# Optimization experiments

Hardware: AMD Instinct MI355X
Metric: run time of the kernel (lower is better)

The kernel has to match this reference:

```python
import jax, jax.numpy as jnp
import numpy as np

BATCH, C_IN, H = 16, 32, 224
N_FILT, K = 64, 5


def setup_inputs() -> dict:
    key = jax.random.key(0)
    k1, k2 = jax.random.split(key)
    x = jax.random.normal(k1, (BATCH, C_IN, H, H), dtype=jnp.float32)
    weight = jax.random.normal(k2, (N_FILT, C_IN, K, K), dtype=jnp.float32)
    bias = jnp.zeros((N_FILT,), dtype=jnp.float32)  # torch init: zeros(1) per filter
    return {"x": x, "weight": weight, "bias": bias}


def reference(x, weight, bias):
    # Fully-connected conv layer: stride 1, VALID padding.
    # Equivalent to stacking per-filter sum(x_patch * w) + scalar bias.
    out = jax.lax.conv_general_dilated(
        x, weight,
        window_strides=(1, 1),
        padding='VALID',
        dimension_numbers=('NCHW', 'OIHW', 'NCHW'),
    )
    # per-filter scalar bias broadcast over spatial dims
    return out + bias[None, :, None, None]
```

## Files before the change

### kernel.cpp

```cpp
#include <hip/hip_runtime.h>

#define CI    32
#define IH    224
#define IW    224
#define OHS   220
#define OWS   220
#define NF    64
#define KS    5

#define XCOLS 228
#define CP    36
#define WPD   40
#define XROWS 8
#define NBUFW (KS * NF * WPD)

#define PXW   116
#define RCHK  (PXW * 4)
#define NROWS 8
#define TCHK  (RCHK * NROWS)
#define ROWB  (RCHK * 16)

typedef __attribute__((ext_vector_type(4))) float   f32x4;
typedef __attribute__((ext_vector_type(4))) __bf16  bf16x4;
typedef __attribute__((ext_vector_type(8))) __bf16  bf16x8;

__global__ void repack_w_kernel(const float* __restrict__ w, __bf16* __restrict__ wp) {
  int i = blockIdx.x * 256 + threadIdx.x;
  if (i >= KS * KS * NF * CI) return;
  int c   = i & (CI - 1);
  int f   = (i >> 5) & (NF - 1);
  int tap = i >> 11;
  int kh = tap / KS, kw = tap % KS;
  wp[i] = (__bf16)w[((f * CI + c) * KS + kh) * KS + kw];
}

__global__ __launch_bounds__(256)
void x_transform(const float* __restrict__ x, __bf16* __restrict__ xh) {
  int chunk = blockIdx.x * 256 + threadIdx.x;
  int c8  = (chunk & 3) * 8;
  int pos = chunk >> 2;
  int w   = pos % IW;
  int nh  = pos / IW;
  int n   = nh / IH;
  int h   = nh - n * IH;
  const float* xp = x + ((size_t)n * CI + c8) * (IH * IW) + h * IW + w;
  bf16x8 v;
#pragma unroll
  for (int j = 0; j < 8; ++j) v[j] = (__bf16)xp[(size_t)j * (IH * IW)];
  *(bf16x8*)(xh + (size_t)pos * CI + c8) = v;
}

__global__ __launch_bounds__(256, 2)
void conv_lds(const __bf16* __restrict__ xh, const __bf16* __restrict__ wp,
              const float* __restrict__ bias, float* __restrict__ out) {
  __shared__ __bf16 xs[TCHK * 8];

  const int tid  = threadIdx.x;
  const int lane = tid & 63;
  const int wv   = tid >> 6;
  const int m    = lane & 15;
  const int q    = lane >> 4;

  const int bid = blockIdx.x;
  const int lid = (bid & 7) * 220 + (bid >> 3);
  const int n   = lid / 110;
  const int rem = lid - n * 110;
  const int oh0 = (rem >> 1) * 4;
  const int ow0 = (rem & 1) * 112;

  {
    const __bf16* xb = xh + (((size_t)n * IH + oh0) * IW + ow0) * CI;
    for (int i = wv; i < TCHK / 64; i += 4) {
      int L  = i * 64 + lane;
      int r  = L / RCHK;
      int cr = L - r * RCHK;
      int cs = cr ^ ((cr >> 3) & 3);
      const __bf16* src = xb + (size_t)r * (IW * CI) + cs * 8;
      __builtin_amdgcn_global_load_lds(
          (const __attribute__((address_space(1))) void*)src,
          (__attribute__((address_space(3))) void*)&xs[i * 512], 16, 0, 0);
    }
  }

  int cj[7], rjv[7];
  int boff[7][5];
#pragma unroll
  for (int j = 0; j < 7; ++j) {
    int t  = wv + j * 4;
    int rj = t / 7;
    rjv[j] = rj;
    cj[j]  = (t - rj * 7) * 16;
#pragma unroll
    for (int kw = 0; kw < KS; ++kw) {
      int g = (cj[j] + kw + m) * 4 + q;
      int s = g ^ ((g >> 3) & 3);
      boff[j][kw] = rj * ROWB + s * 16;
    }
  }

  f32x4 acc[28];
#pragma unroll
  for (int i = 0; i < 28; ++i) { f32x4 z = {0.f, 0.f, 0.f, 0.f}; acc[i] = z; }

  const __bf16* wpl = wp + m * CI + q * 8;

  __syncthreads();

  for (int kh = 0; kh < KS; ++kh) {
    const int khb = kh * ROWB;
#pragma unroll
    for (int kw = 0; kw < KS; ++kw) {
      const int tap = kh * KS + kw;
      bf16x8 af[4];
#pragma unroll
      for (int ft = 0; ft < 4; ++ft)
        af[ft] = *(const bf16x8*)(wpl + (size_t)tap * (NF * CI) + ft * 16 * CI);
#pragma unroll
      for (int j = 0; j < 7; ++j) {
        bf16x8 bv = *(const bf16x8*)((const char*)xs + khb + boff[j][kw]);
#pragma unroll
        for (int ft = 0; ft < 4; ++ft)
          acc[j * 4 + ft] =
              __builtin_amdgcn_mfma_f32_16x16x32_bf16(af[ft], bv, acc[j * 4 + ft], 0, 0, 0);
      }
    }
  }

  float bvv[16];
#pragma unroll
  for (int ft = 0; ft < 4; ++ft)
#pragma unroll
    for (int rg = 0; rg < 4; ++rg)
      bvv[ft * 4 + rg] = bias[ft * 16 + q * 4 + rg];

#pragma unroll
  for (int j = 0; j < 7; ++j) {
    int ow = ow0 + cj[j] + m;
    if (ow < OWS) {
      int oh = oh0 + rjv[j];
#pragma unroll
      for (int ft = 0; ft < 4; ++ft)
#pragma unroll
        for (int rg = 0; rg < 4; ++rg) {
          int f = ft * 16 + q * 4 + rg;
          out[(((size_t)n * NF + f) * OHS + oh) * OWS + ow] = acc[j * 4 + ft][rg] + bvv[ft * 4 + rg];
        }
    }
  }
}

template <bool USE_WS>
__global__ __launch_bounds__(512, 1)
void conv_main(const float* __restrict__ x, const float* __restrict__ w,
               const __bf16* __restrict__ wp, const float* __restrict__ bias,
               float* __restrict__ out) {
  __shared__ __bf16 xs[XROWS * XCOLS * CP];
  __shared__ __bf16 wsm[NBUFW];

  const int tid  = threadIdx.x;
  const int lane = tid & 63;
  const int wv   = tid >> 6;
  const int m    = lane & 15;
  const int q    = lane >> 4;

  int bid = blockIdx.x;
  int lid = (bid >> 3) + (bid & 7) * 110;
  const int n   = lid / 55;
  const int oh0 = (lid % 55) * 4;

  {
    const float* xn = x + (size_t)n * CI * IH * IW;
    for (int p = tid; p < XROWS * 56 * 8; p += 512) {
      int pc   = p & 7;
      int pg   = p >> 3;
      int pcol = pg % 56;
      int prow = pg / 56;
      int row  = oh0 + prow;
      f32x4 v0 = *(const f32x4*)(xn + ((size_t)(pc * 4 + 0) * IH + row) * IW + pcol * 4);
      f32x4 v1 = *(const f32x4*)(xn + ((size_t)(pc * 4 + 1) * IH + row) * IW + pcol * 4);
      f32x4 v2 = *(const f32x4*)(xn + ((size_t)(pc * 4 + 2) * IH + row) * IW + pcol * 4);
      f32x4 v3 = *(const f32x4*)(xn + ((size_t)(pc * 4 + 3) * IH + row) * IW + pcol * 4);
#pragma unroll
      for (int dcol = 0; dcol < 4; ++dcol) {
        bf16x4 t;
        t[0] = (__bf16)v0[dcol]; t[1] = (__bf16)v1[dcol];
        t[2] = (__bf16)v2[dcol]; t[3] = (__bf16)v3[dcol];
        *(bf16x4*)&xs[(prow * XCOLS + pcol * 4 + dcol) * CP + pc * 4] = t;
      }
    }
    for (int z = tid; z < XROWS * 4 * CP; z += 512) {
      int rr  = z / (4 * CP);
      int rem = z - rr * (4 * CP);
      xs[(rr * XCOLS + 224) * CP + rem] = (__bf16)0.0f;
    }
  }

  if (USE_WS) {
    for (int i = tid; i < NF * CI * KS / 8; i += 512) {
      int c0 = (i & 3) * 8;
      int f  = (i >> 2) & 63;
      int kw = i >> 8;
      bf16x8 v = *(const bf16x8*)(wp + ((size_t)(0 * KS + kw) * NF + f) * CI + c0);
      *(bf16x8*)&wsm[(kw * NF + f) * WPD + c0] = v;
    }
  } else {
    for (int i = tid; i < KS * NF * CI; i += 512) {
      int c  = i & 31;
      int f  = (i >> 5) & 63;
      int kw = i >> 11;
      wsm[(kw * NF + f) * WPD + c] = (__bf16)w[((f * CI + c) * KS + 0) * KS + kw];
    }
  }
  __syncthreads();

  int rj[7], cbj[7], xoff[7];
#pragma unroll
  for (int j = 0; j < 7; ++j) {
    int t   = wv + j * 8;
    rj[j]   = t / 14;
    cbj[j]  = (t % 14) * 16;
    xoff[j] = (rj[j] * XCOLS + cbj[j] + m) * CP + q * 8;
  }

  f32x4 acc[28];
#pragma unroll
  for (int i = 0; i < 28; ++i) { f32x4 z = {0.f, 0.f, 0.f, 0.f}; acc[i] = z; }

  for (int kh = 0; kh < KS; ++kh) {
    bf16x8 pw[3];
    if (USE_WS && kh < KS - 1) {
#pragma unroll
      for (int it = 0; it < 3; ++it) {
        int e = it * 512 + tid;
        if (e < 1280) {
          int c0 = (e & 3) * 8;
          int f  = (e >> 2) & 63;
          int kw = e >> 8;
          pw[it] = *(const bf16x8*)(wp + ((size_t)((kh + 1) * KS + kw) * NF + f) * CI + c0);
        }
      }
    }

#pragma unroll
    for (int kw = 0; kw < KS; ++kw) {
      bf16x8 af[4];
#pragma unroll
      for (int ft = 0; ft < 4; ++ft)
        af[ft] = *(const bf16x8*)&wsm[(kw * NF + ft * 16 + m) * WPD + q * 8];
#pragma unroll
      for (int j = 0; j < 7; ++j) {
        const __bf16* bp = &xs[xoff[j] + (kh * XCOLS + kw) * CP];
        bf16x4 lo = *(const bf16x4*)bp;
        bf16x4 hi = *(const bf16x4*)(bp + 4);
        bf16x8 bv8 = __builtin_shufflevector(lo, hi, 0, 1, 2, 3, 4, 5, 6, 7);
#pragma unroll
        for (int ft = 0; ft < 4; ++ft)
          acc[j * 4 + ft] =
              __builtin_amdgcn_mfma_f32_16x16x32_bf16(af[ft], bv8, acc[j * 4 + ft], 0, 0, 0);
      }
    }

    if (kh < KS - 1) {
      __syncthreads();
      if (USE_WS) {
#pragma unroll
        for (int it = 0; it < 3; ++it) {
          int e = it * 512 + tid;
          if (e < 1280) {
            int c0 = (e & 3) * 8;
            int f  = (e >> 2) & 63;
            int kw = e >> 8;
            *(bf16x8*)&wsm[(kw * NF + f) * WPD + c0] = pw[it];
          }
        }
      } else {
        for (int i = tid; i < KS * NF * CI; i += 512) {
          int c  = i & 31;
          int f  = (i >> 5) & 63;
          int kw = i >> 11;
          wsm[(kw * NF + f) * WPD + c] =
              (__bf16)w[((f * CI + c) * KS + (kh + 1)) * KS + kw];
        }
      }
      __syncthreads();
    }
  }

  float bvv[16];
#pragma unroll
  for (int ft = 0; ft < 4; ++ft)
#pragma unroll
    for (int rg = 0; rg < 4; ++rg)
      bvv[ft * 4 + rg] = bias[ft * 16 + q * 4 + rg];

#pragma unroll
  for (int j = 0; j < 7; ++j) {
    int ow = cbj[j] + m;
    if (ow < OWS) {
      int oh = oh0 + rj[j];
#pragma unroll
      for (int ft = 0; ft < 4; ++ft) {
#pragma unroll
        for (int rg = 0; rg < 4; ++rg) {
          int f = ft * 16 + q * 4 + rg;
          out[(((size_t)n * NF + f) * OHS + oh) * OWS + ow] = acc[j * 4 + ft][rg] + bvv[ft * 4 + rg];
        }
      }
    }
  }
}

extern "C" void kernel_launch(void* const* d_in, const int* in_sizes, int n_in,
                              void* d_out, int out_size, void* d_ws, size_t ws_size,
                              hipStream_t stream) {
  const float* x    = (const float*)d_in[0];
  const float* w    = (const float*)d_in[1];
  const float* bias = (const float*)d_in[2];
  float* out = (float*)d_out;

  const int    NW = KS * KS * NF * CI;
  const size_t WB = (size_t)NW * sizeof(__bf16);
  const size_t XB = (size_t)16 * IH * IW * CI * sizeof(__bf16);

  if (ws_size >= XB + WB) {
    __bf16* xhp = (__bf16*)d_ws;
    __bf16* wp  = (__bf16*)((char*)d_ws + XB);
    repack_w_kernel<<<(NW + 255) / 256, 256, 0, stream>>>(w, wp);
    x_transform<<<(16 * IH * IW * 4) / 256, 256, 0, stream>>>(x, xhp);
    conv_lds<<<1760, 256, 0, stream>>>(xhp, wp, bias, out);
  } else if (ws_size >= WB) {
    __bf16* wp = (__bf16*)d_ws;
    repack_w_kernel<<<(NW + 255) / 256, 256, 0, stream>>>(w, wp);
    conv_main<true><<<880, 512, 0, stream>>>(x, w, wp, bias, out);
  } else {
    conv_main<false><<<880, 512, 0, stream>>>(x, w, nullptr, bias, out);
  }
}
```

Before: 360.4 us.

## Fuse weight repack into x transform and shrink conv tiles for 3 blocks/CU

Merges the weight repack and the NHWC bf16 input transform into one prep kernel, removing one launch. The conv kernel now handles 3 output rows per block (7 input rows in LDS instead of 8) with 24 accumulators, aiming for 3 resident blocks per CU. The LDS XOR swizzle is dropped in favour of straight row-wise loads. In exchange, input halo rows are reloaded more often per output, waves get uneven work (6 vs 5 tiles), and LDS bank conflicts may come back without the swizzle.

```diff
diff --git a/kernel.cpp b/kernel.cpp
--- a/kernel.cpp
+++ b/kernel.cpp
@@ -16,13 +16,143 @@
 
 #define PXW   116
 #define RCHK  (PXW * 4)
-#define NROWS 8
-#define TCHK  (RCHK * NROWS)
+#define SROWS 7
 #define ROWB  (RCHK * 16)
 
 typedef __attribute__((ext_vector_type(4))) float   f32x4;
 typedef __attribute__((ext_vector_type(4))) __bf16  bf16x4;
 typedef __attribute__((ext_vector_type(8))) __bf16  bf16x8;
+
+__global__ __launch_bounds__(256)
+void prep_kernel(const float* __restrict__ x, const float* __restrict__ w,
+                 __bf16* __restrict__ xh, __bf16* __restrict__ wp) {
+  int chunk = blockIdx.x * 256 + threadIdx.x;
+  int c8  = (chunk & 3) * 8;
+  int pos = chunk >> 2;
+  int ww  = pos % IW;
+  int nh  = pos / IW;
+  int n   = nh / IH;
+  int h   = nh - n * IH;
+  const float* xp = x + ((size_t)n * CI + c8) * (IH * IW) + h * IW + ww;
+  bf16x8 v;
+#pragma unroll
+  for (int j = 0; j < 8; ++j) v[j] = (__bf16)xp[(size_t)j * (IH * IW)];
+  *(bf16x8*)(xh + (size_t)pos * CI + c8) = v;
+
+  if (blockIdx.x < 200) {
+    int i = blockIdx.x * 256 + threadIdx.x;
+    int c   = i & (CI - 1);
+    int f   = (i >> 5) & (NF - 1);
+    int tap = i >> 11;
+    int kh = tap / KS, kw = tap % KS;
+    wp[i] = (__bf16)w[((f * CI + c) * KS + kh) * KS + kw];
+  }
+}
+
+__global__ __launch_bounds__(256, 3)
+void conv_lds3(const __bf16* __restrict__ xh, const __bf16* __restrict__ wp,
+               const float* __restrict__ bias, float* __restrict__ out) {
+  __shared__ __bf16 xs[SROWS * RCHK * 8];
+
+  const int tid  = threadIdx.x;
+  const int lane = tid & 63;
+  const int wv   = tid >> 6;
+  const int m    = lane & 15;
+  const int q    = lane >> 4;
+
+  const int bid = blockIdx.x;
+  const int lid = (bid & 7) * 296 + (bid >> 3);
+  const int n   = lid / 148;
+  const int rem = lid - n * 148;
+  const int oh0 = (rem >> 1) * 3;
+  const int ow0 = (rem & 1) * 112;
+
+  {
+    const __bf16* xb = xh + (((size_t)n * IH + oh0) * IW + ow0) * CI;
+#pragma unroll
+    for (int rr = 0; rr < 2; ++rr) {
+      int r = wv + rr * 4;
+      if (r < SROWS) {
+        const __bf16* src = xb + (size_t)r * (IW * CI);
+        const int db = r * (RCHK * 8);
+#pragma unroll
+        for (int k = 0; k < 7; ++k)
+          __builtin_amdgcn_global_load_lds(
+              (const __attribute__((address_space(1))) void*)(src + k * 512 + lane * 8),
+              (__attribute__((address_space(3))) void*)&xs[db + k * 512], 16, 0, 0);
+        if (lane < 16)
+          __builtin_amdgcn_global_load_lds(
+              (const __attribute__((address_space(1))) void*)(src + 448 * 8 + lane * 8),
+              (__attribute__((address_space(3))) void*)&xs[db + 448 * 8], 16, 0, 0);
+      }
+    }
+  }
+
+  const int NJ = (wv == 0) ? 6 : 5;
+  int cj[6], rjv[6], bbase[6];
+#pragma unroll
+  for (int j = 0; j < 6; ++j) {
+    int t  = wv + j * 4;
+    int rj = t / 7;
+    rjv[j] = rj;
+    cj[j]  = (t - rj * 7) * 16;
+    bbase[j] = rj * ROWB + ((cj[j] + m) * 4 + q) * 16;
+  }
+
+  f32x4 acc[24];
+#pragma unroll
+  for (int i = 0; i < 24; ++i) { f32x4 z = {0.f, 0.f, 0.f, 0.f}; acc[i] = z; }
+
+  const __bf16* wpl = wp + m * CI + q * 8;
+
+  __syncthreads();
+
+  for (int kh = 0; kh < KS; ++kh) {
+    const int khb = kh * ROWB;
+#pragma unroll
+    for (int kw = 0; kw < KS; ++kw) {
+      bf16x8 af[4];
+#pragma unroll
+      for (int ft = 0; ft < 4; ++ft)
+        af[ft] = *(const bf16x8*)(wpl + (size_t)(kh * KS + kw) * (NF * CI) + ft * 16 * CI);
+#pragma unroll
+      for (int j = 0; j < 6; ++j) {
+        if (j < NJ) {
+          bf16x8 bv = *(const bf16x8*)((const char*)xs + khb + bbase[j] + kw * 64);
+#pragma unroll
+          for (int ft = 0; ft < 4; ++ft)
+            acc[j * 4 + ft] =
+                __builtin_amdgcn_mfma_f32_16x16x32_bf16(af[ft], bv, acc[j * 4 + ft], 0, 0, 0);
+        }
+      }
+    }
+  }
+
+  float bvv[16];
+#pragma unroll
+  for (int ft = 0; ft < 4; ++ft)
+#pragma unroll
+    for (int rg = 0; rg < 4; ++rg)
+      bvv[ft * 4 + rg] = bias[ft * 16 + q * 4 + rg];
+
+#pragma unroll
+  for (int j = 0; j < 6; ++j) {
+    if (j < NJ) {
+      int ow = ow0 + cj[j] + m;
+      int oh = oh0 + rjv[j];
+      if (ow < OWS && oh < OHS) {
+#pragma unroll
+        for (int ft = 0; ft < 4; ++ft)
+#pragma unroll
+          for (int rg = 0; rg < 4; ++rg) {
+            int f = ft * 16 + q * 4 + rg;
+            out[(((size_t)n * NF + f) * OHS + oh) * OWS + ow] =
+                acc[j * 4 + ft][rg] + bvv[ft * 4 + rg];
+          }
+      }
+    }
+  }
+}
 
 __global__ void repack_w_kernel(const float* __restrict__ w, __bf16* __restrict__ wp) {
   int i = blockIdx.x * 256 + threadIdx.x;
@@ -32,121 +162,6 @@
   int tap = i >> 11;
   int kh = tap / KS, kw = tap % KS;
   wp[i] = (__bf16)w[((f * CI + c) * KS + kh) * KS + kw];
-}
-
-__global__ __launch_bounds__(256)
-void x_transform(const float* __restrict__ x, __bf16* __restrict__ xh) {
-  int chunk = blockIdx.x * 256 + threadIdx.x;
-  int c8  = (chunk & 3) * 8;
-  int pos = chunk >> 2;
-  int w   = pos % IW;
-  int nh  = pos / IW;
-  int n   = nh / IH;
-  int h   = nh - n * IH;
-  const float* xp = x + ((size_t)n * CI + c8) * (IH * IW) + h * IW + w;
-  bf16x8 v;
-#pragma unroll
-  for (int j = 0; j < 8; ++j) v[j] = (__bf16)xp[(size_t)j * (IH * IW)];
-  *(bf16x8*)(xh + (size_t)pos * CI + c8) = v;
-}
-
-__global__ __launch_bounds__(256, 2)
-void conv_lds(const __bf16* __restrict__ xh, const __bf16* __restrict__ wp,
-              const float* __restrict__ bias, float* __restrict__ out) {
-  __shared__ __bf16 xs[TCHK * 8];
-
-  const int tid  = threadIdx.x;
-  const int lane = tid & 63;
-  const int wv   = tid >> 6;
-  const int m    = lane & 15;
-  const int q    = lane >> 4;
-
-  const int bid = blockIdx.x;
-  const int lid = (bid & 7) * 220 + (bid >> 3);
-  const int n   = lid / 110;
-  const int rem = lid - n * 110;
-  const int oh0 = (rem >> 1) * 4;
-  const int ow0 = (rem & 1) * 112;
-
-  {
-    const __bf16* xb = xh + (((size_t)n * IH + oh0) * IW + ow0) * CI;
-    for (int i = wv; i < TCHK / 64; i += 4) {
-      int L  = i * 64 + lane;
-      int r  = L / RCHK;
-      int cr = L - r * RCHK;
-      int cs = cr ^ ((cr >> 3) & 3);
-      const __bf16* src = xb + (size_t)r * (IW * CI) + cs * 8;
-      __builtin_amdgcn_global_load_lds(
-          (const __attribute__((address_space(1))) void*)src,
-          (__attribute__((address_space(3))) void*)&xs[i * 512], 16, 0, 0);
-    }
-  }
-
-  int cj[7], rjv[7];
-  int boff[7][5];
-#pragma unroll
-  for (int j = 0; j < 7; ++j) {
-    int t  = wv + j * 4;
-    int rj = t / 7;
-    rjv[j] = rj;
-    cj[j]  = (t - rj * 7) * 16;
-#pragma unroll
-    for (int kw = 0; kw < KS; ++kw) {
-      int g = (cj[j] + kw + m) * 4 + q;
-      int s = g ^ ((g >> 3) & 3);
-      boff[j][kw] = rj * ROWB + s * 16;
-    }
-  }
-
-  f32x4 acc[28];
-#pragma unroll
-  for (int i = 0; i < 28; ++i) { f32x4 z = {0.f, 0.f, 0.f, 0.f}; acc[i] = z; }
-
-  const __bf16* wpl = wp + m * CI + q * 8;
-
-  __syncthreads();
-
-  for (int kh = 0; kh < KS; ++kh) {
-    const int khb = kh * ROWB;
-#pragma unroll
-    for (int kw = 0; kw < KS; ++kw) {
-      const int tap = kh * KS + kw;
-      bf16x8 af[4];
-#pragma unroll
-      for (int ft = 0; ft < 4; ++ft)
-        af[ft] = *(const bf16x8*)(wpl + (size_t)tap * (NF * CI) + ft * 16 * CI);
-#pragma unroll
-      for (int j = 0; j < 7; ++j) {
-        bf16x8 bv = *(const bf16x8*)((const char*)xs + khb + boff[j][kw]);
-#pragma unroll
-        for (int ft = 0; ft < 4; ++ft)
-          acc[j * 4 + ft] =
-              __builtin_amdgcn_mfma_f32_16x16x32_bf16(af[ft], bv, acc[j * 4 + ft], 0, 0, 0);
-      }
-    }
-  }
-
-  float bvv[16];
-#pragma unroll
-  for (int ft = 0; ft < 4; ++ft)
-#pragma unroll
-    for (int rg = 0; rg < 4; ++rg)
-      bvv[ft * 4 + rg] = bias[ft * 16 + q * 4 + rg];
-
-#pragma unroll
-  for (int j = 0; j < 7; ++j) {
-    int ow = ow0 + cj[j] + m;
-    if (ow < OWS) {
-      int oh = oh0 + rjv[j];
-#pragma unroll
-      for (int ft = 0; ft < 4; ++ft)
-#pragma unroll
-        for (int rg = 0; rg < 4; ++rg) {
-          int f = ft * 16 + q * 4 + rg;
-          out[(((size_t)n * NF + f) * OHS + oh) * OWS + ow] = acc[j * 4 + ft][rg] + bvv[ft * 4 + rg];
-        }
-    }
-  }
 }
 
 template <bool USE_WS>
@@ -325,9 +340,8 @@
   if (ws_size >= XB + WB) {
     __bf16* xhp = (__bf16*)d_ws;
     __bf16* wp  = (__bf16*)((char*)d_ws + XB);
-    repack_w_kernel<<<(NW + 255) / 256, 256, 0, stream>>>(w, wp);
-    x_transform<<<(16 * IH * IW * 4) / 256, 256, 0, stream>>>(x, xhp);
-    conv_lds<<<1760, 256, 0, stream>>>(xhp, wp, bias, out);
+    prep_kernel<<<(16 * IH * IW * 4) / 256, 256, 0, stream>>>(x, w, xhp, wp);
+    conv_lds3<<<2368, 256, 0, stream>>>(xhp, wp, bias, out);
   } else if (ws_size >= WB) {
     __bf16* wp = (__bf16*)d_ws;
     repack_w_kernel<<<(NW + 255) / 256, 256, 0, stream>>>(w, wp);
```

Result: slower. 394.9 us (+9.6%).
